# Performance work log

Hardware: AMD Instinct MI355X
Metric: run time of the kernel (lower is better)

The kernel has to match this reference:

```python
import jax, jax.numpy as jnp
import numpy as np

ALPHA = 0.1


def setup_inputs() -> dict:
    key = jax.random.key(0)
    ks = jax.random.split(key, 12)
    B, C, Q, XD, YD, E, H = 4, 256, 256, 64, 32, 64, 128
    inp = {
        "x": jax.random.normal(ks[0], (B, C, XD), jnp.float32),
        "y": jax.random.normal(ks[1], (B, C, YD), jnp.float32),
        "r_c": jax.random.normal(ks[2], (B, C, C, E), jnp.float32),
        "r_q": jax.random.normal(ks[3], (B, C, Q, E), jnp.float32),
        "c_att_map": jax.random.uniform(ks[4], (B, C, C), jnp.float32),
        "q_att_map": jax.random.uniform(ks[5], (B, Q, C), jnp.float32),
        "W1": jax.random.normal(ks[6], (XD + YD + E, H), jnp.float32) * 0.05,
        "b1": jnp.zeros((H,), jnp.float32),
        "W2": jax.random.normal(ks[7], (H, H), jnp.float32) * 0.05,
        "b2": jnp.zeros((H,), jnp.float32),
        "W3": jax.random.normal(ks[8], (H, E), jnp.float32) * 0.05,
        "b3": jnp.zeros((E,), jnp.float32),
    }
    return inp


def reference(x, y, r_c, r_q, c_att_map, q_att_map, W1, b1, W2, b2, W3, b3):
    B, C = r_c.shape[0], r_c.shape[1]
    # tile x,y across an outer C axis and concat with pairwise embeddings
    xx = jnp.broadcast_to(x[:, None, :, :], (B, C, C, x.shape[-1]))
    yy = jnp.broadcast_to(y[:, None, :, :], (B, C, C, y.shape[-1]))
    h = jnp.concatenate([xx, yy, r_c], axis=-1)          # [B,C,C,XD+YD+E]
    h = jax.nn.relu(h @ W1 + b1)
    h = jax.nn.relu(h @ W2 + b2)
    U = h @ W3 + b3                                       # [B,C,C,E]
    # delta[b,k,i,e] = sum_j c_att_map[b,i,j] * U[b,k,j,e]
    delta_r_c = jnp.einsum("bij,bkje->bkie", c_att_map, U)
    delta_r_q = jnp.einsum("bqj,bkje->bkqe", q_att_map, U)
    next_r_c = r_c - ALPHA * delta_r_c
    next_r_q = r_q - ALPHA * delta_r_q
    return (next_r_c, next_r_q)
```

## Files before the change

kernel.cpp:

```cpp
#include <hip/hip_runtime.h>
#include <hip/hip_bf16.h>

typedef __attribute__((ext_vector_type(8))) short  short8;
typedef __attribute__((ext_vector_type(4))) float  f32x4;

#define ALPHA 0.1f

__device__ __forceinline__ unsigned short f2bf(float f) {
    unsigned int u = __float_as_uint(f);
    u = (u + 0x7FFFu + ((u >> 16) & 1u)) >> 16;
    return (unsigned short)u;
}

__device__ __forceinline__ f32x4 mfma16(short8 a, short8 b, f32x4 c) {
    return __builtin_amdgcn_mfma_f32_16x16x32_bf16(a, b, c, 0, 0, 0);
}

#define WS_P     0u
#define WS_W1RT  524288u
#define WS_W2T   540672u
#define WS_W3T   573440u
#define WS_ATTC  589824u
#define WS_ATTQ  1114112u

__global__ __launch_bounds__(256) void prep_kernel(
    const float* __restrict__ x, const float* __restrict__ y,
    const float* __restrict__ cat, const float* __restrict__ qat,
    const float* __restrict__ W1, const float* __restrict__ b1,
    const float* __restrict__ W2, const float* __restrict__ W3,
    unsigned char* __restrict__ ws)
{
    unsigned int t = blockIdx.x * 256u + threadIdx.x;
    float* P = (float*)(ws + WS_P);
    unsigned short* W1rT = (unsigned short*)(ws + WS_W1RT);
    unsigned short* W2T  = (unsigned short*)(ws + WS_W2T);
    unsigned short* W3T  = (unsigned short*)(ws + WS_W3T);
    unsigned short* AC   = (unsigned short*)(ws + WS_ATTC);
    unsigned short* AQ   = (unsigned short*)(ws + WS_ATTQ);

    if (t < 131072u) {
        unsigned int h = t & 127u, bj = t >> 7;
        float acc = b1[h];
        const float* xp = x + bj * 64u;
        const float* yp = y + bj * 32u;
        #pragma unroll 8
        for (int d = 0; d < 64; ++d) acc += xp[d] * W1[d * 128 + h];
        #pragma unroll 8
        for (int d = 0; d < 32; ++d) acc += yp[d] * W1[(64 + d) * 128 + h];
        P[t] = acc;
    } else if (t < 139264u) {
        unsigned int w = t - 131072u, h = w >> 6, e = w & 63u;
        W1rT[w] = f2bf(W1[(96u + e) * 128u + h]);
    } else if (t < 155648u) {
        unsigned int w = t - 139264u, n = w >> 7, k2 = w & 127u;
        W2T[w] = f2bf(W2[k2 * 128u + n]);
    } else if (t < 163840u) {
        unsigned int w = t - 155648u, e = w >> 7, h = w & 127u;
        W3T[w] = f2bf(W3[h * 64u + e]);
    } else if (t < 425984u) {
        unsigned int w = t - 163840u;
        AC[w] = f2bf(cat[w]);
    } else if (t < 688128u) {
        unsigned int w = t - 425984u;
        AQ[w] = f2bf(qat[w]);
    }
}

__global__ __launch_bounds__(256) void fused_kernel(
    const float* __restrict__ rc, const float* __restrict__ rq,
    const float* __restrict__ b2, const float* __restrict__ b3,
    const unsigned char* __restrict__ ws,
    float* __restrict__ out_rc, float* __restrict__ out_rq)
{
    const float* P = (const float*)(ws + WS_P);
    const unsigned short* W1rT = (const unsigned short*)(ws + WS_W1RT);
    const unsigned short* W2T  = (const unsigned short*)(ws + WS_W2T);
    const unsigned short* W3T  = (const unsigned short*)(ws + WS_W3T);
    const unsigned short* AC   = (const unsigned short*)(ws + WS_ATTC);
    const unsigned short* AQ   = (const unsigned short*)(ws + WS_ATTQ);

    __shared__ unsigned short sH[64][136];
    __shared__ unsigned short sUT[64][264];

    const int tid  = threadIdx.x;
    const int lane = tid & 63;
    const int wid  = tid >> 6;
    const int l15  = lane & 15;
    const int lg   = lane >> 4;
    const int b    = blockIdx.y;
    const int k    = blockIdx.x;

    const size_t bk = (size_t)(b * 256 + k);
    const float* rcb = rc + bk * (256 * 64);
    const float* rqb = rq + bk * (256 * 64);
    const float* Pb  = P + b * (256 * 128);

    float b2v[8], b3v[4];
    #pragma unroll
    for (int ct = 0; ct < 8; ++ct) b2v[ct] = b2[16 * ct + l15];
    #pragma unroll
    for (int ct = 0; ct < 4; ++ct) b3v[ct] = b3[16 * ct + l15];

    for (int jc = 0; jc < 4; ++jc) {
        const int jbase = jc * 64 + 16 * wid;

        f32x4 accA[8];
        #pragma unroll
        for (int ct = 0; ct < 8; ++ct) accA[ct] = (f32x4)0.f;
        #pragma unroll
        for (int ks = 0; ks < 2; ++ks) {
            const float* ap = rcb + (jbase + l15) * 64 + 32 * ks + 8 * lg;
            f32x4 a0 = *(const f32x4*)ap;
            f32x4 a1 = *(const f32x4*)(ap + 4);
            short8 af;
            #pragma unroll
            for (int i = 0; i < 4; ++i) {
                af[i]     = (short)f2bf(a0[i]);
                af[4 + i] = (short)f2bf(a1[i]);
            }
            #pragma unroll
            for (int ct = 0; ct < 8; ++ct) {
                short8 bf = *(const short8*)(W1rT + (16 * ct + l15) * 64 + 32 * ks + 8 * lg);
                accA[ct] = mfma16(af, bf, accA[ct]);
            }
        }
        #pragma unroll
        for (int ct = 0; ct < 8; ++ct) {
            #pragma unroll
            for (int r = 0; r < 4; ++r) {
                int j = jbase + 4 * lg + r;
                float v = accA[ct][r] + Pb[j * 128 + 16 * ct + l15];
                v = fmaxf(v, 0.f);
                sH[16 * wid + 4 * lg + r][16 * ct + l15] = f2bf(v);
            }
        }

        f32x4 accB[8];
        #pragma unroll
        for (int ct = 0; ct < 8; ++ct) accB[ct] = (f32x4)0.f;
        #pragma unroll
        for (int ks = 0; ks < 4; ++ks) {
            short8 af = *(const short8*)(&sH[16 * wid + l15][32 * ks + 8 * lg]);
            #pragma unroll
            for (int ct = 0; ct < 8; ++ct) {
                short8 bf = *(const short8*)(W2T + (16 * ct + l15) * 128 + 32 * ks + 8 * lg);
                accB[ct] = mfma16(af, bf, accB[ct]);
            }
        }
        #pragma unroll
        for (int ct = 0; ct < 8; ++ct) {
            #pragma unroll
            for (int r = 0; r < 4; ++r) {
                float v = accB[ct][r] + b2v[ct];
                v = fmaxf(v, 0.f);
                sH[16 * wid + 4 * lg + r][16 * ct + l15] = f2bf(v);
            }
        }

        f32x4 accC[4];
        #pragma unroll
        for (int ct = 0; ct < 4; ++ct) accC[ct] = (f32x4)0.f;
        #pragma unroll
        for (int ks = 0; ks < 4; ++ks) {
            short8 af = *(const short8*)(&sH[16 * wid + l15][32 * ks + 8 * lg]);
            #pragma unroll
            for (int ct = 0; ct < 4; ++ct) {
                short8 bf = *(const short8*)(W3T + (16 * ct + l15) * 128 + 32 * ks + 8 * lg);
                accC[ct] = mfma16(af, bf, accC[ct]);
            }
        }
        #pragma unroll
        for (int ct = 0; ct < 4; ++ct) {
            #pragma unroll
            for (int r = 0; r < 4; ++r) {
                float v = accC[ct][r] + b3v[ct];
                sUT[16 * ct + l15][jc * 64 + 16 * wid + 4 * lg + r] = f2bf(v);
            }
        }
    }

    __syncthreads();

    const unsigned short* acb = AC + b * 65536;
    const unsigned short* aqb = AQ + b * 65536;
    const int i0 = 64 * wid;

    {
        f32x4 acc[4][4];
        #pragma unroll
        for (int rt = 0; rt < 4; ++rt)
            #pragma unroll
            for (int ct = 0; ct < 4; ++ct) acc[rt][ct] = (f32x4)0.f;
        for (int ks = 0; ks < 8; ++ks) {
            short8 bfr[4];
            #pragma unroll
            for (int ct = 0; ct < 4; ++ct)
                bfr[ct] = *(const short8*)(&sUT[16 * ct + l15][32 * ks + 8 * lg]);
            #pragma unroll
            for (int rt = 0; rt < 4; ++rt) {
                short8 af = *(const short8*)(acb + (i0 + 16 * rt + l15) * 256 + 32 * ks + 8 * lg);
                #pragma unroll
                for (int ct = 0; ct < 4; ++ct)
                    acc[rt][ct] = mfma16(af, bfr[ct], acc[rt][ct]);
            }
        }
        #pragma unroll
        for (int rt = 0; rt < 4; ++rt) {
            #pragma unroll
            for (int ct = 0; ct < 4; ++ct) {
                #pragma unroll
                for (int r = 0; r < 4; ++r) {
                    int i = i0 + 16 * rt + 4 * lg + r;
                    int e = 16 * ct + l15;
                    size_t off = bk * 16384 + i * 64 + e;
                    out_rc[off] = rcb[i * 64 + e] - ALPHA * acc[rt][ct][r];
                }
            }
        }
    }

    {
        f32x4 acc[4][4];
        #pragma unroll
        for (int rt = 0; rt < 4; ++rt)
            #pragma unroll
            for (int ct = 0; ct < 4; ++ct) acc[rt][ct] = (f32x4)0.f;
        for (int ks = 0; ks < 8; ++ks) {
            short8 bfr[4];
            #pragma unroll
            for (int ct = 0; ct < 4; ++ct)
                bfr[ct] = *(const short8*)(&sUT[16 * ct + l15][32 * ks + 8 * lg]);
            #pragma unroll
            for (int rt = 0; rt < 4; ++rt) {
                short8 af = *(const short8*)(aqb + (i0 + 16 * rt + l15) * 256 + 32 * ks + 8 * lg);
                #pragma unroll
                for (int ct = 0; ct < 4; ++ct)
                    acc[rt][ct] = mfma16(af, bfr[ct], acc[rt][ct]);
            }
        }
        #pragma unroll
        for (int rt = 0; rt < 4; ++rt) {
            #pragma unroll
            for (int ct = 0; ct < 4; ++ct) {
                #pragma unroll
                for (int r = 0; r < 4; ++r) {
                    int i = i0 + 16 * rt + 4 * lg + r;
                    int e = 16 * ct + l15;
                    size_t off = bk * 16384 + i * 64 + e;
                    out_rq[off] = rqb[i * 64 + e] - ALPHA * acc[rt][ct][r];
                }
            }
        }
    }
}

extern "C" void kernel_launch(void* const* d_in, const int* in_sizes, int n_in,
                              void* d_out, int out_size, void* d_ws, size_t ws_size,
                              hipStream_t stream)
{
    const float* x   = (const float*)d_in[0];
    const float* y   = (const float*)d_in[1];
    const float* rc  = (const float*)d_in[2];
    const float* rq  = (const float*)d_in[3];
    const float* cat = (const float*)d_in[4];
    const float* qat = (const float*)d_in[5];
    const float* W1  = (const float*)d_in[6];
    const float* b1  = (const float*)d_in[7];
    const float* W2  = (const float*)d_in[8];
    const float* b2  = (const float*)d_in[9];
    const float* W3  = (const float*)d_in[10];
    const float* b3  = (const float*)d_in[11];

    float* out_rc = (float*)d_out;
    float* out_rq = out_rc + (size_t)4 * 256 * 256 * 64;
    unsigned char* ws = (unsigned char*)d_ws;

    prep_kernel<<<2688, 256, 0, stream>>>(x, y, cat, qat, W1, b1, W2, W3, ws);
    fused_kernel<<<dim3(256, 4), 256, 0, stream>>>(rc, rq, b2, b3, ws, out_rc, out_rq);
}
```

Before: 369.9 us.

## Swap MFMA operand roles so fragments store as contiguous vectors

Swaps the A and B operands of every MFMA so each lane's four accumulator values lie along a contiguous feature or embedding dimension. Intermediate LDS writes become 4-element short vectors, and the final rc/rq reads and output writes become float4 accesses instead of scattered scalar ones. The prep kernel now converts the attention maps four elements per thread with vector loads, and the main kernel gets a launch-bounds occupancy hint of three blocks. The aim is to cut memory transactions on the bandwidth-heavy output path, at the risk of register pressure from the occupancy hint.

```diff
diff --git a/kernel.cpp b/kernel.cpp
--- a/kernel.cpp
+++ b/kernel.cpp
@@ -2,6 +2,7 @@
 #include <hip/hip_bf16.h>
 
 typedef __attribute__((ext_vector_type(8))) short  short8;
+typedef __attribute__((ext_vector_type(4))) short  short4v;
 typedef __attribute__((ext_vector_type(4))) float  f32x4;
 
 #define ALPHA 0.1f
@@ -30,7 +31,7 @@
     const float* __restrict__ W2, const float* __restrict__ W3,
     unsigned char* __restrict__ ws)
 {
-    unsigned int t = blockIdx.x * 256u + threadIdx.x;
+    const unsigned int blk = blockIdx.x, tid = threadIdx.x;
     float* P = (float*)(ws + WS_P);
     unsigned short* W1rT = (unsigned short*)(ws + WS_W1RT);
     unsigned short* W2T  = (unsigned short*)(ws + WS_W2T);
@@ -38,7 +39,8 @@
     unsigned short* AC   = (unsigned short*)(ws + WS_ATTC);
     unsigned short* AQ   = (unsigned short*)(ws + WS_ATTQ);
 
-    if (t < 131072u) {
+    if (blk < 512u) {
+        unsigned int t = blk * 256u + tid;
         unsigned int h = t & 127u, bj = t >> 7;
         float acc = b1[h];
         const float* xp = x + bj * 64u;
@@ -48,25 +50,36 @@
         #pragma unroll 8
         for (int d = 0; d < 32; ++d) acc += yp[d] * W1[(64 + d) * 128 + h];
         P[t] = acc;
-    } else if (t < 139264u) {
-        unsigned int w = t - 131072u, h = w >> 6, e = w & 63u;
+    } else if (blk < 544u) {
+        unsigned int w = (blk - 512u) * 256u + tid;
+        unsigned int h = w >> 6, e = w & 63u;
         W1rT[w] = f2bf(W1[(96u + e) * 128u + h]);
-    } else if (t < 155648u) {
-        unsigned int w = t - 139264u, n = w >> 7, k2 = w & 127u;
+    } else if (blk < 608u) {
+        unsigned int w = (blk - 544u) * 256u + tid;
+        unsigned int n = w >> 7, k2 = w & 127u;
         W2T[w] = f2bf(W2[k2 * 128u + n]);
-    } else if (t < 163840u) {
-        unsigned int w = t - 155648u, e = w >> 7, h = w & 127u;
+    } else if (blk < 640u) {
+        unsigned int w = (blk - 608u) * 256u + tid;
+        unsigned int e = w >> 7, h = w & 127u;
         W3T[w] = f2bf(W3[h * 64u + e]);
-    } else if (t < 425984u) {
-        unsigned int w = t - 163840u;
-        AC[w] = f2bf(cat[w]);
-    } else if (t < 688128u) {
-        unsigned int w = t - 425984u;
-        AQ[w] = f2bf(qat[w]);
+    } else if (blk < 896u) {
+        unsigned int w = (blk - 640u) * 256u + tid;
+        f32x4 v = *(const f32x4*)(cat + 4u * w);
+        short4v o;
+        #pragma unroll
+        for (int i = 0; i < 4; ++i) o[i] = (short)f2bf(v[i]);
+        *(short4v*)(AC + 4u * w) = o;
+    } else {
+        unsigned int w = (blk - 896u) * 256u + tid;
+        f32x4 v = *(const f32x4*)(qat + 4u * w);
+        short4v o;
+        #pragma unroll
+        for (int i = 0; i < 4; ++i) o[i] = (short)f2bf(v[i]);
+        *(short4v*)(AQ + 4u * w) = o;
     }
 }
 
-__global__ __launch_bounds__(256) void fused_kernel(
+__global__ __launch_bounds__(256, 3) void fused_kernel(
     const float* __restrict__ rc, const float* __restrict__ rq,
     const float* __restrict__ b2, const float* __restrict__ b3,
     const unsigned char* __restrict__ ws,
@@ -95,66 +108,63 @@
     const float* rqb = rq + bk * (256 * 64);
     const float* Pb  = P + b * (256 * 128);
 
-    float b2v[8], b3v[4];
-    #pragma unroll
-    for (int ct = 0; ct < 8; ++ct) b2v[ct] = b2[16 * ct + l15];
+    float b3v[4];
     #pragma unroll
     for (int ct = 0; ct < 4; ++ct) b3v[ct] = b3[16 * ct + l15];
 
     for (int jc = 0; jc < 4; ++jc) {
-        const int jbase = jc * 64 + 16 * wid;
+        const int jrow = jc * 64 + 16 * wid + l15;
 
         f32x4 accA[8];
         #pragma unroll
-        for (int ct = 0; ct < 8; ++ct) accA[ct] = (f32x4)0.f;
+        for (int mt = 0; mt < 8; ++mt) accA[mt] = (f32x4)0.f;
         #pragma unroll
         for (int ks = 0; ks < 2; ++ks) {
-            const float* ap = rcb + (jbase + l15) * 64 + 32 * ks + 8 * lg;
+            const float* ap = rcb + jrow * 64 + 32 * ks + 8 * lg;
             f32x4 a0 = *(const f32x4*)ap;
             f32x4 a1 = *(const f32x4*)(ap + 4);
-            short8 af;
+            short8 bfrag;
             #pragma unroll
             for (int i = 0; i < 4; ++i) {
-                af[i]     = (short)f2bf(a0[i]);
-                af[4 + i] = (short)f2bf(a1[i]);
-            }
-            #pragma unroll
-            for (int ct = 0; ct < 8; ++ct) {
-                short8 bf = *(const short8*)(W1rT + (16 * ct + l15) * 64 + 32 * ks + 8 * lg);
-                accA[ct] = mfma16(af, bf, accA[ct]);
-            }
-        }
-        #pragma unroll
-        for (int ct = 0; ct < 8; ++ct) {
-            #pragma unroll
-            for (int r = 0; r < 4; ++r) {
-                int j = jbase + 4 * lg + r;
-                float v = accA[ct][r] + Pb[j * 128 + 16 * ct + l15];
-                v = fmaxf(v, 0.f);
-                sH[16 * wid + 4 * lg + r][16 * ct + l15] = f2bf(v);
-            }
+                bfrag[i]     = (short)f2bf(a0[i]);
+                bfrag[4 + i] = (short)f2bf(a1[i]);
+            }
+            #pragma unroll
+            for (int mt = 0; mt < 8; ++mt) {
+                short8 afrag = *(const short8*)(W1rT + (16 * mt + l15) * 64 + 32 * ks + 8 * lg);
+                accA[mt] = mfma16(afrag, bfrag, accA[mt]);
+            }
+        }
+        #pragma unroll
+        for (int mt = 0; mt < 8; ++mt) {
+            f32x4 p4 = *(const f32x4*)(Pb + jrow * 128 + 16 * mt + 4 * lg);
+            short4v o;
+            #pragma unroll
+            for (int r = 0; r < 4; ++r)
+                o[r] = (short)f2bf(fmaxf(accA[mt][r] + p4[r], 0.f));
+            *(short4v*)&sH[16 * wid + l15][16 * mt + 4 * lg] = o;
         }
 
         f32x4 accB[8];
         #pragma unroll
-        for (int ct = 0; ct < 8; ++ct) accB[ct] = (f32x4)0.f;
+        for (int mt = 0; mt < 8; ++mt) accB[mt] = (f32x4)0.f;
         #pragma unroll
         for (int ks = 0; ks < 4; ++ks) {
-            short8 af = *(const short8*)(&sH[16 * wid + l15][32 * ks + 8 * lg]);
-            #pragma unroll
-            for (int ct = 0; ct < 8; ++ct) {
-                short8 bf = *(const short8*)(W2T + (16 * ct + l15) * 128 + 32 * ks + 8 * lg);
-                accB[ct] = mfma16(af, bf, accB[ct]);
-            }
-        }
-        #pragma unroll
-        for (int ct = 0; ct < 8; ++ct) {
-            #pragma unroll
-            for (int r = 0; r < 4; ++r) {
-                float v = accB[ct][r] + b2v[ct];
-                v = fmaxf(v, 0.f);
-                sH[16 * wid + 4 * lg + r][16 * ct + l15] = f2bf(v);
-            }
+            short8 bfrag = *(const short8*)(&sH[16 * wid + l15][32 * ks + 8 * lg]);
+            #pragma unroll
+            for (int mt = 0; mt < 8; ++mt) {
+                short8 afrag = *(const short8*)(W2T + (16 * mt + l15) * 128 + 32 * ks + 8 * lg);
+                accB[mt] = mfma16(afrag, bfrag, accB[mt]);
+            }
+        }
+        #pragma unroll
+        for (int mt = 0; mt < 8; ++mt) {
+            f32x4 b2q = *(const f32x4*)(b2 + 16 * mt + 4 * lg);
+            short4v o;
+            #pragma unroll
+            for (int r = 0; r < 4; ++r)
+                o[r] = (short)f2bf(fmaxf(accB[mt][r] + b2q[r], 0.f));
+            *(short4v*)&sH[16 * wid + l15][16 * mt + 4 * lg] = o;
         }
 
         f32x4 accC[4];
@@ -162,93 +172,62 @@
         for (int ct = 0; ct < 4; ++ct) accC[ct] = (f32x4)0.f;
         #pragma unroll
         for (int ks = 0; ks < 4; ++ks) {
-            short8 af = *(const short8*)(&sH[16 * wid + l15][32 * ks + 8 * lg]);
+            short8 afrag = *(const short8*)(&sH[16 * wid + l15][32 * ks + 8 * lg]);
             #pragma unroll
             for (int ct = 0; ct < 4; ++ct) {
-                short8 bf = *(const short8*)(W3T + (16 * ct + l15) * 128 + 32 * ks + 8 * lg);
-                accC[ct] = mfma16(af, bf, accC[ct]);
+                short8 bfrag = *(const short8*)(W3T + (16 * ct + l15) * 128 + 32 * ks + 8 * lg);
+                accC[ct] = mfma16(afrag, bfrag, accC[ct]);
             }
         }
         #pragma unroll
         for (int ct = 0; ct < 4; ++ct) {
-            #pragma unroll
-            for (int r = 0; r < 4; ++r) {
-                float v = accC[ct][r] + b3v[ct];
-                sUT[16 * ct + l15][jc * 64 + 16 * wid + 4 * lg + r] = f2bf(v);
-            }
+            short4v o;
+            #pragma unroll
+            for (int r = 0; r < 4; ++r)
+                o[r] = (short)f2bf(accC[ct][r] + b3v[ct]);
+            *(short4v*)&sUT[16 * ct + l15][jc * 64 + 16 * wid + 4 * lg] = o;
         }
     }
 
     __syncthreads();
 
-    const unsigned short* acb = AC + b * 65536;
-    const unsigned short* aqb = AQ + b * 65536;
+    const unsigned short* amap[2] = { AC + b * 65536, AQ + b * 65536 };
+    const float* src[2]           = { rcb, rqb };
+    float* dst[2] = { out_rc + bk * 16384, out_rq + bk * 16384 };
     const int i0 = 64 * wid;
 
-    {
+    #pragma unroll
+    for (int p = 0; p < 2; ++p) {
         f32x4 acc[4][4];
         #pragma unroll
-        for (int rt = 0; rt < 4; ++rt)
-            #pragma unroll
-            for (int ct = 0; ct < 4; ++ct) acc[rt][ct] = (f32x4)0.f;
+        for (int et = 0; et < 4; ++et)
+            #pragma unroll
+            for (int it = 0; it < 4; ++it) acc[et][it] = (f32x4)0.f;
         for (int ks = 0; ks < 8; ++ks) {
-            short8 bfr[4];
-            #pragma unroll
-            for (int ct = 0; ct < 4; ++ct)
-                bfr[ct] = *(const short8*)(&sUT[16 * ct + l15][32 * ks + 8 * lg]);
-            #pragma unroll
-            for (int rt = 0; rt < 4; ++rt) {
-                short8 af = *(const short8*)(acb + (i0 + 16 * rt + l15) * 256 + 32 * ks + 8 * lg);
+            short8 uf[4];
+            #pragma unroll
+            for (int et = 0; et < 4; ++et)
+                uf[et] = *(const short8*)(&sUT[16 * et + l15][32 * ks + 8 * lg]);
+            #pragma unroll
+            for (int it = 0; it < 4; ++it) {
+                short8 af = *(const short8*)(amap[p] + (i0 + 16 * it + l15) * 256 + 32 * ks + 8 * lg);
                 #pragma unroll
-                for (int ct = 0; ct < 4; ++ct)
-                    acc[rt][ct] = mfma16(af, bfr[ct], acc[rt][ct]);
-            }
-        }
-        #pragma unroll
-        for (int rt = 0; rt < 4; ++rt) {
-            #pragma unroll
-            for (int ct = 0; ct < 4; ++ct) {
+                for (int et = 0; et < 4; ++et)
+                    acc[et][it] = mfma16(uf[et], af, acc[et][it]);
+            }
+        }
+        #pragma unroll
+        for (int it = 0; it < 4; ++it) {
+            #pragma unroll
+            for (int et = 0; et < 4; ++et) {
+                const int i = i0 + 16 * it + l15;
+                const int e0 = 16 * et + 4 * lg;
+                f32x4 rv = *(const f32x4*)(src[p] + i * 64 + e0);
+                f32x4 o;
                 #pragma unroll
-                for (int r = 0; r < 4; ++r) {
-                    int i = i0 + 16 * rt + 4 * lg + r;
-                    int e = 16 * ct + l15;
-                    size_t off = bk * 16384 + i * 64 + e;
-                    out_rc[off] = rcb[i * 64 + e] - ALPHA * acc[rt][ct][r];
-                }
-            }
-        }
-    }
-
-    {
-        f32x4 acc[4][4];
-        #pragma unroll
-        for (int rt = 0; rt < 4; ++rt)
-            #pragma unroll
-            for (int ct = 0; ct < 4; ++ct) acc[rt][ct] = (f32x4)0.f;
-        for (int ks = 0; ks < 8; ++ks) {
-            short8 bfr[4];
-            #pragma unroll
-            for (int ct = 0; ct < 4; ++ct)
-                bfr[ct] = *(const short8*)(&sUT[16 * ct + l15][32 * ks + 8 * lg]);
-            #pragma unroll
-            for (int rt = 0; rt < 4; ++rt) {
-                short8 af = *(const short8*)(aqb + (i0 + 16 * rt + l15) * 256 + 32 * ks + 8 * lg);
-                #pragma unroll
-                for (int ct = 0; ct < 4; ++ct)
-                    acc[rt][ct] = mfma16(af, bfr[ct], acc[rt][ct]);
-            }
-        }
-        #pragma unroll
-        for (int rt = 0; rt < 4; ++rt) {
-            #pragma unroll
-            for (int ct = 0; ct < 4; ++ct) {
-                #pragma unroll
-                for (int r = 0; r < 4; ++r) {
-                    int i = i0 + 16 * rt + 4 * lg + r;
-                    int e = 16 * ct + l15;
-                    size_t off = bk * 16384 + i * 64 + e;
-                    out_rq[off] = rqb[i * 64 + e] - ALPHA * acc[rt][ct][r];
-                }
+                for (int r = 0; r < 4; ++r)
+                    o[r] = rv[r] - ALPHA * acc[et][it][r];
+                *(f32x4*)(dst[p] + i * 64 + e0) = o;
             }
         }
     }
@@ -275,6 +254,6 @@
     float* out_rq = out_rc + (size_t)4 * 256 * 256 * 64;
     unsigned char* ws = (unsigned char*)d_ws;
 
-    prep_kernel<<<2688, 256, 0, stream>>>(x, y, cat, qat, W1, b1, W2, W3, ws);
+    prep_kernel<<<1152, 256, 0, stream>>>(x, y, cat, qat, W1, b1, W2, W3, ws);
     fused_kernel<<<dim3(256, 4), 256, 0, stream>>>(rc, rq, b2, b3, ws, out_rc, out_rq);
 }
```

After: 534.2 us. 1.44x slower.
